# Optimization experiments

Hardware: AMD Instinct MI355X
Metric: run time of the kernel (lower is better)

## Reference

```python
import jax, jax.numpy as jnp
import numpy as np

HAD_BLOCK = 128
HAD_SCALE = 2.0 ** (-3.5)  # 1/sqrt(128), orthonormal block Hadamard


def _hadamard_matrix(n):
    H = np.array([[1.0]], dtype=np.float32)
    while H.shape[0] < n:
        H = np.block([[H, H], [H, -H]])
    return jnp.asarray(H)

_H = _hadamard_matrix(HAD_BLOCK)


def hadamard_transform(x, scale):
    # x: (..., D) with D % 128 == 0; blockwise Hadamard rotation on last dim
    shp = x.shape
    xb = x.reshape(shp[:-1] + (shp[-1] // HAD_BLOCK, HAD_BLOCK))
    y = jnp.einsum('...b,cb->...c', xb, _H) * scale
    return y.reshape(shp)


def setup_inputs() -> dict:
    key = jax.random.key(0)
    kx, kw, kb = jax.random.split(key, 3)
    B, S, IN, OUT = 4, 2048, 4096, 4096
    x = jax.random.normal(kx, (B, S, IN), dtype=jnp.float32)
    # master fp weight, then preprocess: Hadamard-rotate rows, quantize to int4,
    # pack two nibbles per element (per-out-channel scale/add)
    w = jax.random.normal(kw, (OUT, IN), dtype=jnp.float32) / np.float32(np.sqrt(IN))
    w_had = hadamard_transform(w, HAD_SCALE)
    wmin = w_had.min(axis=1, keepdims=True)
    wmax = w_had.max(axis=1, keepdims=True)
    w_scale = jnp.maximum((wmax - wmin) / 15.0, 1e-8)  # [OUT,1]
    w_add = wmin                                        # [OUT,1]
    w_int = jnp.clip(jnp.round((w_had - w_add) / w_scale), 0, 15).astype(jnp.int32)
    w_int_packed = (w_int[:, ::2] | (w_int[:, 1::2] << 4)).astype(jnp.int32)  # [OUT, IN//2]
    bias = jax.random.normal(kb, (OUT,), dtype=jnp.float32) * 0.01
    return {"x": x, "w_int_packed": w_int_packed, "w_scale": w_scale,
            "w_add": w_add, "bias": bias}


def reference(x, w_int_packed, w_scale, w_add, bias):
    OUT = w_int_packed.shape[0]
    IN = w_int_packed.shape[1] * 2
    # unpack int4 nibbles -> [OUT, IN]
    low = w_int_packed & 0xF
    high = (w_int_packed >> 4) & 0xF
    w_int = jnp.stack([low, high], axis=-1).reshape(OUT, IN).astype(w_scale.dtype)
    # per-out-channel dequant
    w_deq = w_int * w_scale + w_add  # [OUT, IN]
    # fused Hadamard rotation on activations (matches rotated weight)
    a = hadamard_transform(x, HAD_SCALE)  # [B,S,IN]
    y = jnp.einsum('bsi,oi->bso', a, w_deq)
    return y + bias
```

## Files before the change

### kernel.cpp

```cpp
#include <hip/hip_runtime.h>
#include <hip/hip_bf16.h>
#include <hip/hip_fp16.h>

#define IN_DIM 4096
#define OUT_DIM 4096
#define HAD_SCALE_F 0.08838834764831845f

typedef int   i32x4 __attribute__((ext_vector_type(4)));
typedef float f32x4 __attribute__((ext_vector_type(4)));

__global__ __launch_bounds__(256)
void had_rows_q(const float* __restrict__ x, int* __restrict__ aq,
                float* __restrict__ rowsum, float* __restrict__ srow)
{
    __shared__ float lds[IN_DIM];
    __shared__ float wmx[4];
    __shared__ int   wqs[4];
    const int tid = threadIdx.x;
    const size_t row = blockIdx.x;
    const float* xr = x + row * IN_DIM;

    #pragma unroll
    for (int v = 0; v < 4; ++v) {
        const int idx = v * 1024 + tid * 4;
        *(float4*)&lds[idx] = *(const float4*)&xr[idx];
    }
    __syncthreads();

    #pragma unroll
    for (int s = 0; s < 7; ++s) {
        const int stride = 1 << s;
        #pragma unroll
        for (int t = 0; t < 8; ++t) {
            const int p   = t * 256 + tid;
            const int blk = p >> 6;
            const int q   = p & 63;
            const int i   = ((q & ~(stride - 1)) << 1) | (q & (stride - 1));
            const int lo  = blk * 128 + i;
            const float u  = lds[lo];
            const float v2 = lds[lo + stride];
            lds[lo]          = u + v2;
            lds[lo + stride] = u - v2;
        }
        __syncthreads();
    }

    float e[16];
    float smax = 0.f;
    #pragma unroll
    for (int v = 0; v < 4; ++v) {
        const int idx = v * 1024 + tid * 4;
        const float4 f = *(const float4*)&lds[idx];
        e[v*4+0] = f.x * HAD_SCALE_F; e[v*4+1] = f.y * HAD_SCALE_F;
        e[v*4+2] = f.z * HAD_SCALE_F; e[v*4+3] = f.w * HAD_SCALE_F;
        smax = fmaxf(smax, fmaxf(fmaxf(fabsf(e[v*4+0]), fabsf(e[v*4+1])),
                                 fmaxf(fabsf(e[v*4+2]), fabsf(e[v*4+3]))));
    }
    #pragma unroll
    for (int off = 32; off > 0; off >>= 1)
        smax = fmaxf(smax, __shfl_down(smax, off, 64));
    if ((tid & 63) == 0) wmx[tid >> 6] = smax;
    __syncthreads();
    const float mx  = fmaxf(fmaxf(wmx[0], wmx[1]), fmaxf(wmx[2], wmx[3]));
    const float inv = (mx > 0.f) ? 127.0f / mx : 0.f;
    const float sa  = mx * (1.0f / 127.0f);

    int qsum = 0;
    #pragma unroll
    for (int v = 0; v < 4; ++v) {
        const int idx = v * 1024 + tid * 4;
        const int q0 = (int)rintf(e[v*4+0] * inv);
        const int q1 = (int)rintf(e[v*4+1] * inv);
        const int q2 = (int)rintf(e[v*4+2] * inv);
        const int q3 = (int)rintf(e[v*4+3] * inv);
        qsum += (q0 + q1) + (q2 + q3);
        aq[(row * IN_DIM + idx) >> 2] =
            (q0 & 0xFF) | ((q1 & 0xFF) << 8) | ((q2 & 0xFF) << 16) | (q3 << 24);
    }
    #pragma unroll
    for (int off = 32; off > 0; off >>= 1) qsum += __shfl_down(qsum, off, 64);
    if ((tid & 63) == 0) wqs[tid >> 6] = qsum;
    __syncthreads();
    if (tid == 0) {
        rowsum[row] = sa * (float)((wqs[0] + wqs[1]) + (wqs[2] + wqs[3]));
        srow[row]   = sa;
    }
}

__global__ __launch_bounds__(256)
void unpack_w8(const int* __restrict__ wp, signed char* __restrict__ wf8)
{
    const int gid = blockIdx.x * 256 + threadIdx.x;
    const int n   = gid >> 9;
    const int k0  = (gid & 511) * 8;
    const int4 p  = *(const int4*)(wp + (size_t)n * (IN_DIM / 2) + (k0 >> 1));
    const unsigned lo = (unsigned)(p.x & 15) | ((unsigned)((p.x >> 4) & 15) << 8)
                      | ((unsigned)(p.y & 15) << 16) | ((unsigned)((p.y >> 4) & 15) << 24);
    const unsigned hi = (unsigned)(p.z & 15) | ((unsigned)((p.z >> 4) & 15) << 8)
                      | ((unsigned)(p.w & 15) << 16) | ((unsigned)((p.w >> 4) & 15) << 24);
    *(uint2*)(wf8 + (size_t)n * IN_DIM + k0) = make_uint2(lo, hi);
}

#define NT (IN_DIM / 128)
#define NI (NT / 2)

#define BAR()        asm volatile("s_barrier" ::: "memory")
#define WAIT_VM(N)   asm volatile("s_waitcnt vmcnt(" #N ")" ::: "memory")

#define STAGE_A(p, R, kt) __builtin_amdgcn_global_load_lds( \
    (const __attribute__((address_space(1))) void*)(sA + (((size_t)(R)) << 18) + (((size_t)((kt) & 31)) << 7)), \
    (__attribute__((address_space(3))) void*)(smem + (p) * 65536 + (R) * 8192 + dstA), 16, 0, 0)
#define STAGE_B(p, R, kt) __builtin_amdgcn_global_load_lds( \
    (const __attribute__((address_space(1))) void*)(sB + (((size_t)(R)) << 18) + (((size_t)((kt) & 31)) << 7)), \
    (__attribute__((address_space(3))) void*)(smem + (p) * 65536 + (R) * 8192 + dstB), 16, 0, 0)

#define LDA(p, mq, mi, kb) (*(const i32x4*)(smem + (p)*65536 + (mq)*8192 + (mi)*2048 + aOffK[kb]))
#define LDB(p, nq, ni, kb) (*(const i32x4*)(smem + (p)*65536 + (nq)*4096 + (ni)*2048 + bOffK[kb]))

#define LOAD_A_TO(dst, p, mq) do { \
    _Pragma("unroll") for (int mi = 0; mi < 4; ++mi) { \
        dst[mi][0] = LDA(p, mq, mi, 0); \
        dst[mi][1] = LDA(p, mq, mi, 1); \
    } } while (0)

#define LOAD_B(p, nq) do { \
    _Pragma("unroll") for (int ni = 0; ni < 2; ++ni) { \
        bfr[(nq)*2+ni][0] = LDB(p, nq, ni, 0); \
        bfr[(nq)*2+ni][1] = LDB(p, nq, ni, 1); \
    } } while (0)

#define MFMA_Q(abuf, mq, nq) do { \
    __builtin_amdgcn_s_setprio(1); \
    _Pragma("unroll") for (int mi = 0; mi < 4; ++mi) \
    _Pragma("unroll") for (int ni = 0; ni < 2; ++ni) \
    _Pragma("unroll") for (int kb = 0; kb < 2; ++kb) \
        acc[(mq)*4+mi][(nq)*2+ni] = __builtin_amdgcn_mfma_i32_16x16x64_i8( \
            abuf[mi][kb], bfr[(nq)*2+ni][kb], acc[(mq)*4+mi][(nq)*2+ni], 0, 0, 0); \
    __builtin_amdgcn_s_setprio(0); \
} while (0)

__global__ __launch_bounds__(512, 2)
void gemm_i8(const signed char* __restrict__ Aq, const signed char* __restrict__ Bw,
             const float* __restrict__ wscale, const float* __restrict__ wadd,
             const float* __restrict__ bias, const float* __restrict__ rowsum,
             const float* __restrict__ srow, float* __restrict__ out)
{
    __shared__ char smem[131072];

    const int tid  = threadIdx.x;
    const int lane = tid & 63;
    const int w    = tid >> 6;
    const int wm   = w >> 2;
    const int wn   = w & 3;

    const int bid = blockIdx.x;
    const int wg  = (bid & 7) * 64 + (bid >> 3);
    const int m0  = (wg >> 4) * 256;
    const int n0  = (wg & 15) * 256;

    const int rt = tid >> 3;
    const int ct = (tid & 7) ^ (rt & 7);
    const signed char* sA = Aq + (size_t)(m0 + rt) * IN_DIM + ct * 16;
    const signed char* sB = Bw + (size_t)(n0 + rt) * IN_DIM + ct * 16;
    const int dstA = w * 1024;
    const int dstB = 32768 + w * 1024;

    const int l15 = lane & 15, g = lane >> 4, l7 = lane & 7;
    const int s0 = (g ^ l7) << 4;
    int aOffK[2], bOffK[2];
    aOffK[0] = (wm * 128 + l15) * 128 + s0;
    aOffK[1] = (wm * 128 + l15) * 128 + (s0 ^ 64);
    bOffK[0] = 32768 + (wn * 64 + l15) * 128 + s0;
    bOffK[1] = 32768 + (wn * 64 + l15) * 128 + (s0 ^ 64);

    i32x4 afrA[4][2], afrB[4][2], bfr[4][2];
    i32x4 acc[8][4] = {};

    #pragma unroll
    for (int R = 0; R < 4; ++R) { STAGE_A(0, R, 0); STAGE_B(0, R, 0); }
    #pragma unroll
    for (int R = 0; R < 4; ++R) { STAGE_A(1, R, 1); STAGE_B(1, R, 1); }
    WAIT_VM(8);
    BAR();
    LOAD_B(0, 0);
    LOAD_A_TO(afrA, 0, 0);

    #pragma unroll 1
    for (int it = 0; it < NI; ++it) {
        const int kt1 = 2 * it + 1;
        const int kt2 = (2 * it + 2) & (NT - 1);
        const int kt3 = (2 * it + 3) & (NT - 1);

        LOAD_B(0, 1);
        if (it) { STAGE_B(1, 2, kt1); STAGE_B(1, 3, kt1); }
        MFMA_Q(afrA, 0, 0);
        LOAD_A_TO(afrB, 0, 1);
        if (it) { STAGE_A(1, 1, kt1); STAGE_A(1, 3, kt1); }
        MFMA_Q(afrA, 0, 1);
        if (it) { WAIT_VM(2); } else { WAIT_VM(0); }
        BAR();

        STAGE_B(0, 0, kt2); STAGE_B(0, 1, kt2);
        MFMA_Q(afrB, 1, 0);
        LOAD_B(1, 0);
        LOAD_A_TO(afrA, 1, 0);
        STAGE_A(0, 0, kt2); STAGE_A(0, 2, kt2);
        MFMA_Q(afrB, 1, 1);
        WAIT_VM(4);
        BAR();

        STAGE_B(0, 2, kt2); STAGE_B(0, 3, kt2);
        MFMA_Q(afrA, 0, 0);
        LOAD_B(1, 1);
        LOAD_A_TO(afrB, 1, 1);
        STAGE_A(0, 1, kt2); STAGE_A(0, 3, kt2);
        MFMA_Q(afrA, 0, 1);
        WAIT_VM(2);
        BAR();

        STAGE_B(1, 0, kt3); STAGE_B(1, 1, kt3);
        MFMA_Q(afrB, 1, 0);
        LOAD_B(0, 0);
        LOAD_A_TO(afrA, 0, 0);
        STAGE_A(1, 0, kt3); STAGE_A(1, 2, kt3);
        MFMA_Q(afrB, 1, 1);
        WAIT_VM(4);
        BAR();
    }

    #pragma unroll
    for (int n = 0; n < 4; ++n) {
        const int col = n0 + wn * 64 + n * 16 + l15;
        const float sc = wscale[col];
        const float ad = wadd[col];
        const float bi = bias[col];
        #pragma unroll
        for (int m = 0; m < 8; ++m) {
            const int row = m0 + wm * 128 + m * 16 + g * 4;
            const float4 rs4 = *(const float4*)&rowsum[row];
            const float4 sr4 = *(const float4*)&srow[row];
            #pragma unroll
            for (int j = 0; j < 4; ++j) {
                const float rs = (j == 0) ? rs4.x : (j == 1) ? rs4.y : (j == 2) ? rs4.z : rs4.w;
                const float sr = (j == 0) ? sr4.x : (j == 1) ? sr4.y : (j == 2) ? sr4.z : sr4.w;
                out[(size_t)(row + j) * OUT_DIM + col] =
                    (float)acc[m][n][j] * (sc * sr) + ad * rs + bi;
            }
        }
    }
}

extern "C" void kernel_launch(void* const* d_in, const int* in_sizes, int n_in,
                              void* d_out, int out_size, void* d_ws, size_t ws_size,
                              hipStream_t stream)
{
    const float* x      = (const float*)d_in[0];
    const int*   wp     = (const int*)d_in[1];
    const float* wscale = (const float*)d_in[2];
    const float* wadd   = (const float*)d_in[3];
    const float* bias   = (const float*)d_in[4];
    float*       out    = (float*)d_out;

    const int M = in_sizes[0] / IN_DIM;

    char* ws = (char*)d_ws;
    signed char* wf8 = (signed char*)ws;
    const size_t wf_bytes = (size_t)OUT_DIM * IN_DIM;
    int* aq = (int*)(ws + wf_bytes);
    const size_t aq_bytes = (size_t)M * IN_DIM;
    float* rowsum = (float*)(ws + wf_bytes + aq_bytes);
    float* srow   = (float*)(ws + wf_bytes + aq_bytes + (size_t)M * 4);

    const int unpack_blocks = (OUT_DIM * (IN_DIM / 8)) / 256;
    unpack_w8<<<unpack_blocks, 256, 0, stream>>>(wp, wf8);

    had_rows_q<<<M, 256, 0, stream>>>(x, aq, rowsum, srow);

    gemm_i8<<<(M / 256) * (OUT_DIM / 256), 512, 0, stream>>>(
        (const signed char*)aq, wf8, wscale, wadd, bias, rowsum, srow, out);
}
```

Measured before the change: 194.7 us.

## Restructure int8 GEMM register fragment schedule with separate B-fragment buffers

Splits the B fragment register array into three named buffers and reorders the LDS-to-register fragment loads so each phase issues its loads before the MFMA blocks instead of between them. Global-to-LDS staging is grouped together ahead of the MFMAs. The aim is to hide LDS read latency behind matrix instructions and avoid stalls where an MFMA waits on a freshly loaded fragment. The cost is more live vector registers, which may pressure occupancy at two blocks per CU, and the barrier ordering must still keep reads of a buffer ahead of overwrites of it.

After: 261.0 us. 34.1% more time.

```diff
diff --git a/kernel.cpp b/kernel.cpp
--- a/kernel.cpp
+++ b/kernel.cpp
@@ -123,19 +123,19 @@
         dst[mi][1] = LDA(p, mq, mi, 1); \
     } } while (0)
 
-#define LOAD_B(p, nq) do { \
+#define LOAD_B_TO(dst, p, nq) do { \
     _Pragma("unroll") for (int ni = 0; ni < 2; ++ni) { \
-        bfr[(nq)*2+ni][0] = LDB(p, nq, ni, 0); \
-        bfr[(nq)*2+ni][1] = LDB(p, nq, ni, 1); \
+        dst[ni][0] = LDB(p, nq, ni, 0); \
+        dst[ni][1] = LDB(p, nq, ni, 1); \
     } } while (0)
 
-#define MFMA_Q(abuf, mq, nq) do { \
+#define MFMA_Q2(abuf, bset, mq, nq) do { \
     __builtin_amdgcn_s_setprio(1); \
     _Pragma("unroll") for (int mi = 0; mi < 4; ++mi) \
     _Pragma("unroll") for (int ni = 0; ni < 2; ++ni) \
     _Pragma("unroll") for (int kb = 0; kb < 2; ++kb) \
         acc[(mq)*4+mi][(nq)*2+ni] = __builtin_amdgcn_mfma_i32_16x16x64_i8( \
-            abuf[mi][kb], bfr[(nq)*2+ni][kb], acc[(mq)*4+mi][(nq)*2+ni], 0, 0, 0); \
+            abuf[mi][kb], bset[ni][kb], acc[(mq)*4+mi][(nq)*2+ni], 0, 0, 0); \
     __builtin_amdgcn_s_setprio(0); \
 } while (0)
 
@@ -173,7 +173,8 @@
     bOffK[0] = 32768 + (wn * 64 + l15) * 128 + s0;
     bOffK[1] = 32768 + (wn * 64 + l15) * 128 + (s0 ^ 64);
 
-    i32x4 afrA[4][2], afrB[4][2], bfr[4][2];
+    i32x4 afrA[4][2], afrB[4][2];
+    i32x4 bfr0[2][2], b2A[2][2], b2B[2][2];
     i32x4 acc[8][4] = {};
 
     #pragma unroll
@@ -182,7 +183,8 @@
     for (int R = 0; R < 4; ++R) { STAGE_A(1, R, 1); STAGE_B(1, R, 1); }
     WAIT_VM(8);
     BAR();
-    LOAD_B(0, 0);
+    LOAD_B_TO(bfr0, 0, 0);
+    LOAD_B_TO(b2A, 0, 1);
     LOAD_A_TO(afrA, 0, 0);
 
     #pragma unroll 1
@@ -191,39 +193,39 @@
         const int kt2 = (2 * it + 2) & (NT - 1);
         const int kt3 = (2 * it + 3) & (NT - 1);
 
-        LOAD_B(0, 1);
-        if (it) { STAGE_B(1, 2, kt1); STAGE_B(1, 3, kt1); }
-        MFMA_Q(afrA, 0, 0);
         LOAD_A_TO(afrB, 0, 1);
-        if (it) { STAGE_A(1, 1, kt1); STAGE_A(1, 3, kt1); }
-        MFMA_Q(afrA, 0, 1);
+        if (it) { STAGE_B(1, 2, kt1); STAGE_B(1, 3, kt1);
+                  STAGE_A(1, 1, kt1); STAGE_A(1, 3, kt1); }
+        MFMA_Q2(afrA, bfr0, 0, 0);
+        MFMA_Q2(afrA, b2A, 0, 1);
         if (it) { WAIT_VM(2); } else { WAIT_VM(0); }
         BAR();
 
+        LOAD_A_TO(afrA, 1, 0);
+        LOAD_B_TO(b2B, 1, 1);
         STAGE_B(0, 0, kt2); STAGE_B(0, 1, kt2);
-        MFMA_Q(afrB, 1, 0);
-        LOAD_B(1, 0);
-        LOAD_A_TO(afrA, 1, 0);
         STAGE_A(0, 0, kt2); STAGE_A(0, 2, kt2);
-        MFMA_Q(afrB, 1, 1);
+        MFMA_Q2(afrB, bfr0, 1, 0);
+        LOAD_B_TO(bfr0, 1, 0);
+        MFMA_Q2(afrB, b2A, 1, 1);
         WAIT_VM(4);
         BAR();
 
+        LOAD_A_TO(afrB, 1, 1);
         STAGE_B(0, 2, kt2); STAGE_B(0, 3, kt2);
-        MFMA_Q(afrA, 0, 0);
-        LOAD_B(1, 1);
-        LOAD_A_TO(afrB, 1, 1);
         STAGE_A(0, 1, kt2); STAGE_A(0, 3, kt2);
-        MFMA_Q(afrA, 0, 1);
+        MFMA_Q2(afrA, bfr0, 0, 0);
+        MFMA_Q2(afrA, b2B, 0, 1);
         WAIT_VM(2);
         BAR();
 
+        LOAD_A_TO(afrA, 0, 0);
+        LOAD_B_TO(b2A, 0, 1);
         STAGE_B(1, 0, kt3); STAGE_B(1, 1, kt3);
-        MFMA_Q(afrB, 1, 0);
-        LOAD_B(0, 0);
-        LOAD_A_TO(afrA, 0, 0);
         STAGE_A(1, 0, kt3); STAGE_A(1, 2, kt3);
-        MFMA_Q(afrB, 1, 1);
+        MFMA_Q2(afrB, bfr0, 1, 0);
+        LOAD_B_TO(bfr0, 0, 0);
+        MFMA_Q2(afrB, b2B, 1, 1);
         WAIT_VM(4);
         BAR();
     }
```
